# Kernel optimization log

Measured on AMD Instinct MI355X. Metric: run time of the kernel, lower is better.

## Reference

```python
import jax, jax.numpy as jnp
import numpy as np

N = 100000      # nodes
E = 1600000     # edges
F_IN, H1, H2, H3, F_OUT = 64, 128, 128, 64, 8


def _lin(key, fan_in, fan_out):
    return jax.random.normal(key, (fan_in, fan_out), jnp.float32) / np.sqrt(fan_in).astype(np.float32)


def setup_inputs() -> dict:
    key = jax.random.key(0)
    ks = jax.random.split(key, 16)
    x = jax.random.normal(ks[0], (N, F_IN), jnp.float32)
    edge_index = jax.random.randint(ks[1], (2, E), 0, N, dtype=jnp.int64)
    return {
        "x": x,
        "edge_index": edge_index,
        "eps1": jnp.zeros((), jnp.float32),
        "eps2": jnp.zeros((), jnp.float32),
        "eps3": jnp.zeros((), jnp.float32),
        "W1a": _lin(ks[2], F_IN, H1), "b1a": jnp.zeros((H1,), jnp.float32),
        "W1b": _lin(ks[3], H1, H1),   "b1b": jnp.zeros((H1,), jnp.float32),
        "W2a": _lin(ks[4], H1, H2),   "b2a": jnp.zeros((H2,), jnp.float32),
        "W2b": _lin(ks[5], H2, H2),   "b2b": jnp.zeros((H2,), jnp.float32),
        "W3a": _lin(ks[6], H2, H3),   "b3a": jnp.zeros((H3,), jnp.float32),
        "W3b": _lin(ks[7], H3, H3),   "b3b": jnp.zeros((H3,), jnp.float32),
        "Wfc": _lin(ks[8], H3, F_OUT), "bfc": jnp.zeros((F_OUT,), jnp.float32),
    }


def _gin_conv(x, src, dst, eps, Wa, ba, Wb, bb):
    # out_i = MLP((1+eps) * x_i + sum_{j in N(i)} x_j)
    agg = jax.ops.segment_sum(x[src], dst, num_segments=N)  # scatter-add over edges
    h = (1.0 + eps) * x + agg
    return jax.nn.relu(h @ Wa + ba) @ Wb + bb


def reference(x, edge_index, eps1, eps2, eps3,
              W1a, b1a, W1b, b1b,
              W2a, b2a, W2b, b2b,
              W3a, b3a, W3b, b3b,
              Wfc, bfc):
    src, dst = edge_index[0], edge_index[1]
    x = jax.nn.relu(_gin_conv(x, src, dst, eps1, W1a, b1a, W1b, b1b))
    x = jax.nn.relu(_gin_conv(x, src, dst, eps2, W2a, b2a, W2b, b2b))
    x = jax.nn.relu(_gin_conv(x, src, dst, eps3, W3a, b3a, W3b, b3b))
    emb = jax.lax.stop_gradient(x)  # x.clone().detach()
    out = x @ Wfc + bfc
    return out, emb
```

## Files before the change

kernel.cpp:

```cpp
#include <hip/hip_runtime.h>
#include <hip/hip_bf16.h>
#include <stdint.h>

typedef unsigned short ushort_t;
typedef __attribute__((ext_vector_type(8))) short short8;
typedef __attribute__((ext_vector_type(4))) float floatx4;
typedef __attribute__((ext_vector_type(2))) float floatx2;

__device__ __forceinline__ float bf2f(unsigned short u){
  union { unsigned int i; float f; } v; v.i = ((unsigned int)u) << 16; return v.f;
}
__device__ __forceinline__ unsigned short f2bf(float f){
  union { float f; unsigned int i; } v; v.f = f;
  unsigned int r = v.i + 0x7FFFu + ((v.i >> 16) & 1u);
  return (unsigned short)(r >> 16);
}
__device__ __forceinline__ unsigned int pack2(unsigned short lo, unsigned short hi){
  return ((unsigned int)hi << 16) | (unsigned int)lo;
}
__device__ __forceinline__ float bflo(unsigned int v){
  union { unsigned int u; float f; } c; c.u = v << 16; return c.f;
}
__device__ __forceinline__ float bfhi(unsigned int v){
  union { unsigned int u; float f; } c; c.u = v & 0xffff0000u; return c.f;
}
__device__ __forceinline__ floatx2 bfpair(unsigned int v){
  union { unsigned int u; float f; } lo, hi;
  lo.u = v << 16; hi.u = v & 0xffff0000u;
  floatx2 r; r.x = lo.f; r.y = hi.f; return r;
}


__global__ __launch_bounds__(256)
void k_prep(const unsigned int* __restrict__ w, int* __restrict__ ghist, int E, int N, int nbB,
            const float2* __restrict__ xin, unsigned int* __restrict__ xb, int total2, int tobfB,
            const float* __restrict__ W1a, const float* __restrict__ W1b, const float* __restrict__ W2a,
            const float* __restrict__ W2b, const float* __restrict__ W3a, const float* __restrict__ W3b,
            const float* __restrict__ Wfc, ushort_t* __restrict__ wout)
{
  int b = blockIdx.x, t = threadIdx.x;
  if (b < nbB){
    __shared__ int h[256];
    __shared__ unsigned int dred[4];
    h[t] = 0;
    int base = b*4096 + t;
    unsigned int acc = 0;
    #pragma unroll
    for (int i=0;i<16;++i){
      int e = base + i*256;
      if (e < E) acc |= w[2*e+1];
    }
    #pragma unroll
    for (int o=32;o>=1;o>>=1) acc |= __shfl_xor(acc, o);
    if ((t&63)==0) dred[t>>6] = acc;
    __syncthreads();
    int m = (dred[0]|dred[1]|dred[2]|dred[3]) != 0;
    #pragma unroll
    for (int i=0;i<16;++i){
      int e = base + i*256;
      if (e < E){
        int d = m ? (int)w[(size_t)E + e] : (int)w[2*((size_t)E + e)];
        if ((unsigned)d < (unsigned)N) atomicAdd(&h[d>>9], 1);
      }
    }
    __syncthreads();
    if (h[t]) atomicAdd(&ghist[t], h[t]);
  } else if (b < nbB + tobfB){
    int i = (b - nbB)*256 + t;
    if (i < total2){
      float2 v = xin[i];
      xb[i] = pack2(f2bf(v.x), f2bf(v.y));
    }
  } else {
    int id = (b - nbB - tobfB)*256 + t;
    const float* src; int K, M, base2, local;
    if      (id <  8192){ src=W1a; K=64;  M=128; base2=0;     local=id; }
    else if (id < 24576){ src=W1b; K=128; M=128; base2=8192;  local=id-8192; }
    else if (id < 40960){ src=W2a; K=128; M=128; base2=24576; local=id-24576; }
    else if (id < 57344){ src=W2b; K=128; M=128; base2=40960; local=id-40960; }
    else if (id < 65536){ src=W3a; K=128; M=64;  base2=57344; local=id-57344; }
    else if (id < 69632){ src=W3b; K=64;  M=64;  base2=65536; local=id-65536; }
    else if (id < 70656){ src=Wfc; K=64;  M=16;  base2=69632; local=id-69632; }
    else if (id < 74752){ src=nullptr; K=64; M=64; base2=70656; local=id-70656; }
    else return;
    int k = local / M, nn = local - k*M;
    float val;
    if (src == nullptr) val = (k == nn) ? 1.0f : 0.0f;
    else if (src == Wfc) val = (nn<8) ? Wfc[k*8+nn] : 0.0f;
    else                 val = src[k*M+nn];
    int idx = (((nn>>4)*(K/32) + (k>>5))*4 + ((k>>3)&3))*128 + (nn&15)*8 + (k&7);
    wout[base2+idx] = f2bf(val);
  }
}


__global__ __launch_bounds__(256) void k_bscan(const int* __restrict__ ghist, int* __restrict__ bbase,
                                               int* __restrict__ gcur, int NB){
  __shared__ int sv[256];
  int t = threadIdx.x;
  int v = (t < NB) ? ghist[t] : 0;
  sv[t] = v; __syncthreads();
  for (int o=1;o<256;o<<=1){
    int xv = (t>=o)? sv[t-o] : 0;
    __syncthreads();
    sv[t] += xv;
    __syncthreads();
  }
  int excl = sv[t] - v;
  if (t < NB){ bbase[t] = excl; gcur[t] = excl; }
  if (t == NB-1) bbase[NB] = excl + v;
}

__global__ __launch_bounds__(256) void k_bin(const unsigned int* __restrict__ w,
                                             int* __restrict__ gcur, int2* __restrict__ pairs,
                                             int E, int N, int NB){
  __shared__ int h[256];
  __shared__ int cur[256];
  __shared__ unsigned int dred[4];
  int t = threadIdx.x;
  h[t] = 0;
  int base = blockIdx.x*4096 + t;
  unsigned int acc = 0;
  #pragma unroll
  for (int i=0;i<16;++i){
    int e = base + i*256;
    if (e < E) acc |= w[2*e+1];
  }
  #pragma unroll
  for (int o=32;o>=1;o>>=1) acc |= __shfl_xor(acc, o);
  if ((t&63)==0) dred[t>>6] = acc;
  __syncthreads();
  int m = (dred[0]|dred[1]|dred[2]|dred[3]) != 0;
  int d[16], s[16];
  #pragma unroll
  for (int i=0;i<16;++i){
    int e = base + i*256;
    d[i] = -1; s[i] = 0;
    if (e < E){
      if (m){ s[i] = (int)w[e];           d[i] = (int)w[(size_t)E + e]; }
      else  { s[i] = (int)w[2*(size_t)e]; d[i] = (int)w[2*((size_t)E + e)]; }
      if ((unsigned)d[i] >= (unsigned)N || (unsigned)s[i] >= (unsigned)N) d[i] = -1;
    }
  }
  #pragma unroll
  for (int i=0;i<16;++i)
    if (d[i] >= 0) atomicAdd(&h[d[i]>>9], 1);
  __syncthreads();
  if (t < NB && h[t]) cur[t] = atomicAdd(&gcur[t], h[t]);
  __syncthreads();
  #pragma unroll
  for (int i=0;i<16;++i){
    if (d[i] >= 0){
      int p = atomicAdd(&cur[d[i]>>9], 1);
      pairs[p] = make_int2(d[i], s[i]);
    }
  }
}

__global__ __launch_bounds__(256) void k_bcsr(const int2* __restrict__ pairs, const int* __restrict__ bbase,
                                              int* __restrict__ offs, int* __restrict__ csr, int N, int NB){
  __shared__ int cnt[512];
  __shared__ int wsum[4];
  int b = blockIdx.x, t = threadIdx.x, lane = t&63, wv = t>>6;
  int lo = bbase[b], hi = bbase[b+1];
  int node0 = b << 9;
  cnt[t] = 0; cnt[t+256] = 0;
  __syncthreads();
  for (int i = lo+t; i < hi; i += 256){
    int2 p = pairs[i];
    atomicAdd(&cnt[p.x - node0], 1);
  }
  __syncthreads();
  int v0 = cnt[2*t], v1 = cnt[2*t+1], tot = v0+v1;
  int s = tot;
  #pragma unroll
  for (int o=1;o<64;o<<=1){ int xv = __shfl_up(s,o); if (lane>=o) s += xv; }
  if (lane==63) wsum[wv] = s;
  __syncthreads();
  int basev = 0;
  for (int j=0;j<wv;++j) basev += wsum[j];
  int excl = basev + s - tot;
  int e0 = lo + excl, e1 = lo + excl + v0;
  cnt[2*t] = e0; cnt[2*t+1] = e1;
  int n0 = node0 + 2*t, n1 = node0 + 2*t + 1;
  if (n0 < N) offs[n0] = e0;
  if (n1 < N) offs[n1] = e1;
  if (b == NB-1 && t == 255) offs[N] = hi;
  __syncthreads();
  for (int i = lo+t; i < hi; i += 256){
    int2 p = pairs[i];
    int pos = atomicAdd(&cnt[p.x - node0], 1);
    csr[pos] = p.y;
  }
}


template<int F>
__global__ __launch_bounds__(256) void k_gatherx(const uint4* __restrict__ xr, const int* __restrict__ offs,
                                                 const int* __restrict__ csr, const float* __restrict__ epsp,
                                                 uint4* __restrict__ hr, int n, int nzrow){
  constexpr int RS  = F/8;
  constexpr int LPN = 4*RS;
  constexpr int NPW = 64/LPN;
  constexpr int CH  = LPN;
  constexpr int MAXG = CH/16;
  int gt = blockIdx.x*256 + threadIdx.x;
  int wv = gt >> 6, lane = gt & 63;
  int grp = lane / LPN;
  int lin = lane % LPN;
  int q   = lin / RS;
  int f   = lin % RS;
  int node = wv*NPW + grp;
  if (node >= n) return;
  const size_t row = (size_t)node*RS;
  float e1s = 1.0f + epsp[0];
  floatx2 a0,a1,a2,a3;
  if (q == 0){
    uint4 sv = xr[row + f];
    floatx2 es; es.x = e1s; es.y = e1s;
    a0 = es*bfpair(sv.x); a1 = es*bfpair(sv.y);
    a2 = es*bfpair(sv.z); a3 = es*bfpair(sv.w);
  } else {
    floatx2 z; z.x = 0.f; z.y = 0.f;
    a0 = z; a1 = z; a2 = z; a3 = z;
  }
  int u0 = offs[node], u1 = offs[node+1];
  int deg = u1 - u0;

#define ISSUE(g, V0,V1,V2,V3) { int bb = grp*LPN + (g)*16 + q; \
    int s0=__shfl(cv,bb), s1=__shfl(cv,bb+4), s2=__shfl(cv,bb+8), s3=__shfl(cv,bb+12); \
    V0 = xr[(size_t)s0*RS + f]; V1 = xr[(size_t)s1*RS + f]; \
    V2 = xr[(size_t)s2*RS + f]; V3 = xr[(size_t)s3*RS + f]; }
#define ACCV(V)  { a0 += bfpair((V).x); a1 += bfpair((V).y); a2 += bfpair((V).z); a3 += bfpair((V).w); }
#define ACC4(V0,V1,V2,V3) { ACCV(V0) ACCV(V1) ACCV(V2) ACCV(V3) }

  for (int c0 = 0; c0 < deg; c0 += CH){
    int rem = deg - c0;
    int cv = nzrow;
    if (lin < rem) cv = csr[u0 + c0 + lin];
    int nk = rem < CH ? rem : CH;
    int ng = (nk + 15) >> 4;
    uint4 A0,A1,A2,A3, B0,B1,B2,B3;
    ISSUE(0, A0,A1,A2,A3)
    if (ng > 1) { ISSUE(1, B0,B1,B2,B3) }
    ACC4(A0,A1,A2,A3)
    if (ng > 1){
      if constexpr (MAXG >= 3) { if (ng > 2) ISSUE(2, A0,A1,A2,A3) }
      ACC4(B0,B1,B2,B3)
      if constexpr (MAXG >= 3){
        if (ng > 2){
          if (ng > 3) { ISSUE(3, B0,B1,B2,B3) }
          ACC4(A0,A1,A2,A3)
          if (ng > 3) { ACC4(B0,B1,B2,B3) }
        }
      }
    }
  }
#undef ISSUE
#undef ACCV
#undef ACC4
#define RED(av) { av.x += __shfl_xor(av.x, RS);   av.y += __shfl_xor(av.y, RS); \
                  av.x += __shfl_xor(av.x, 2*RS); av.y += __shfl_xor(av.y, 2*RS); }
  RED(a0) RED(a1) RED(a2) RED(a3)
#undef RED
  if (q == 0){
    uint4 o;
    o.x = pack2(f2bf(a0.x), f2bf(a0.y));
    o.y = pack2(f2bf(a1.x), f2bf(a1.y));
    o.z = pack2(f2bf(a2.x), f2bf(a2.y));
    o.w = pack2(f2bf(a3.x), f2bf(a3.y));
    hr[row + f] = o;
  }
}


template<int F, int M1, int M2, bool LAST, bool Y3>
__global__ __launch_bounds__(256)
void k_mlp(const ushort_t* __restrict__ h,
           const ushort_t* __restrict__ wp1, const float* __restrict__ b1,
           const ushort_t* __restrict__ wp2, const float* __restrict__ b2,
           ushort_t* __restrict__ xout,
           float* __restrict__ embp,
           const ushort_t* __restrict__ wpfc, const float* __restrict__ bfc,
           float* __restrict__ outp, int n)
{
  constexpr int NT1 = M1/16, NT2 = M2/16, KC1 = F/32, KC2 = M1/32;
  __shared__ short sC1[4*(M1/8)*136];
  __shared__ short sX3[LAST ? (4*8*136) : 1];
  int tid = threadIdx.x, lane = tid&63, w = tid>>6;
  int m16 = lane&15, quad = lane>>4;
  int row0 = blockIdx.x*64 + w*16;
  size_t arow = (size_t)(row0 + m16);

  floatx4 acc[NT1];
  #pragma unroll
  for (int i=0;i<NT1;++i) acc[i] = (floatx4){0.f,0.f,0.f,0.f};
  #pragma unroll
  for (int kc=0; kc<KC1; ++kc){
    short8 a = *(const short8*)(h + arow*F + kc*32 + quad*8);
    #pragma unroll
    for (int nt=0; nt<NT1; ++nt){
      short8 b = *(const short8*)(wp1 + (size_t)((nt*KC1+kc)*64 + lane)*8);
      acc[nt] = __builtin_amdgcn_mfma_f32_16x16x32_bf16(a, b, acc[nt], 0, 0, 0);
    }
  }
  #pragma unroll
  for (int nt=0; nt<NT1; ++nt){
    int c = nt*16 + m16;
    float bias = b1[c];
    #pragma unroll
    for (int r=0;r<4;++r){
      float v = fmaxf(acc[nt][r] + bias, 0.f);
      int mm = quad*4 + r;
      sC1[(w*(M1/8) + (c>>3))*136 + mm*8 + (c&7)] = (short)f2bf(v);
    }
  }
  __syncthreads();

  floatx4 acc2[NT2];
  #pragma unroll
  for (int i=0;i<NT2;++i) acc2[i] = (floatx4){0.f,0.f,0.f,0.f};
  #pragma unroll
  for (int kc=0; kc<KC2; ++kc){
    short8 a = *(const short8*)&sC1[(w*(M1/8) + kc*4 + quad)*136 + m16*8];
    #pragma unroll
    for (int nt=0; nt<NT2; ++nt){
      short8 b = *(const short8*)(wp2 + (size_t)((nt*KC2+kc)*64 + lane)*8);
      acc2[nt] = __builtin_amdgcn_mfma_f32_16x16x32_bf16(a, b, acc2[nt], 0, 0, 0);
    }
  }
  #pragma unroll
  for (int nt=0; nt<NT2; ++nt){
    int c = nt*16 + m16;
    float bias = b2[c];
    #pragma unroll
    for (int r=0;r<4;++r){
      float v = fmaxf(acc2[nt][r] + bias, 0.f);
      int mm = quad*4 + r;
      int row = row0 + mm;
      if constexpr (Y3){
        sC1[(w*(M2/8) + (c>>3))*136 + mm*8 + (c&7)] = (short)f2bf(v);
      } else if constexpr (!LAST){
        if (row < n) xout[(size_t)row*M2 + c] = f2bf(v);
      } else {
        if (row < n) embp[(size_t)row*64 + c] = v;
        sX3[(w*8 + (c>>3))*136 + mm*8 + (c&7)] = (short)f2bf(v);
      }
    }
  }

  if constexpr (Y3){
    constexpr int KC3 = M2/32;
    floatx4 acc3[4];
    #pragma unroll
    for (int i=0;i<4;++i) acc3[i] = (floatx4){0.f,0.f,0.f,0.f};
    #pragma unroll
    for (int kc=0; kc<KC3; ++kc){
      short8 a = *(const short8*)&sC1[(w*(M2/8) + kc*4 + quad)*136 + m16*8];
      #pragma unroll
      for (int nt=0; nt<4; ++nt){
        short8 b = *(const short8*)(wpfc + (size_t)((nt*KC3+kc)*64 + lane)*8);
        acc3[nt] = __builtin_amdgcn_mfma_f32_16x16x32_bf16(a, b, acc3[nt], 0, 0, 0);
      }
    }
    #pragma unroll
    for (int nt=0; nt<4; ++nt){
      int c = nt*16 + m16;
      #pragma unroll
      for (int r=0;r<4;++r){
        int row = row0 + quad*4 + r;
        if (row < n) xout[(size_t)row*64 + c] = f2bf(acc3[nt][r]);
      }
    }
  }

  if constexpr (LAST){
    __syncthreads();
    floatx4 accf = (floatx4){0.f,0.f,0.f,0.f};
    #pragma unroll
    for (int kc=0; kc<2; ++kc){
      short8 a = *(const short8*)&sX3[(w*8 + kc*4 + quad)*136 + m16*8];
      short8 b = *(const short8*)(wpfc + (size_t)(kc*64 + lane)*8);
      accf = __builtin_amdgcn_mfma_f32_16x16x32_bf16(a, b, accf, 0, 0, 0);
    }
    if (m16 < 8){
      float bias = bfc[m16];
      #pragma unroll
      for (int r=0;r<4;++r){
        int row = row0 + quad*4 + r;
        if (row < n) outp[(size_t)row*8 + m16] = accf[r] + bias;
      }
    }
  }
}


extern "C" void kernel_launch(void* const* d_in, const int* in_sizes, int n_in,
                              void* d_out, int out_size, void* d_ws, size_t ws_size,
                              hipStream_t stream)
{
  const int N = in_sizes[0] / 64;
  const int E = in_sizes[1] / 2;
  const int NB = (N + 511) / 512;
  const float*        x    = (const float*)d_in[0];
  const unsigned int* ew   = (const unsigned int*)d_in[1];
  const float* eps1 = (const float*)d_in[2];
  const float* eps2 = (const float*)d_in[3];
  const float* eps3 = (const float*)d_in[4];
  const float* W1a  = (const float*)d_in[5];
  const float* b1a  = (const float*)d_in[6];
  const float* W1b  = (const float*)d_in[7];
  const float* b1b  = (const float*)d_in[8];
  const float* W2a  = (const float*)d_in[9];
  const float* b2a  = (const float*)d_in[10];
  const float* W2b  = (const float*)d_in[11];
  const float* b2b  = (const float*)d_in[12];
  const float* W3a  = (const float*)d_in[13];
  const float* b3a  = (const float*)d_in[14];
  const float* W3b  = (const float*)d_in[15];
  const float* b3b  = (const float*)d_in[16];
  const float* Wfc  = (const float*)d_in[17];
  const float* bfc  = (const float*)d_in[18];

  float* outp = (float*)d_out;
  float* emb  = outp + (size_t)N*8;

  const int Npad = ((N + 63)/64)*64;

  char* ws = (char*)d_ws;
  size_t o = 0;
  auto alloc = [&](size_t bytes)->char* {
    char* p = ws + o;
    o = (o + bytes + 255) & ~(size_t)255;
    return p;
  };
  int*      ghist = (int*)alloc(256*4);
  int*      bbase = (int*)alloc(257*4);
  int*      gcur  = (int*)alloc(256*4);
  int*      offs  = (int*)alloc((size_t)(N+1)*4);
  int2*     pairs = (int2*)alloc((size_t)E*8);
  int*      csr   = (int*)alloc((size_t)E*4);
  ushort_t* wperm = (ushort_t*)alloc(74752ull*2);
  ushort_t* xb    = (ushort_t*)alloc(((size_t)Npad + 64)*64*2);
  ushort_t* hbuf  = (ushort_t*)alloc((size_t)Npad*128*2);
  ushort_t* x1    = (ushort_t*)alloc(((size_t)Npad + 64)*128*2);
  ushort_t* ybuf  = (ushort_t*)alloc(((size_t)Npad + 64)*64*2);

  hipMemsetAsync(ghist, 0, 256*4, stream);
  hipMemsetAsync(xb + (size_t)N*64, 0, 64*2, stream);
  hipMemsetAsync(x1 + (size_t)N*128, 0, 128*2, stream);
  hipMemsetAsync(ybuf + (size_t)N*64, 0, 64*2, stream);
  const int nbB   = (E + 4095)/4096;
  const int tobfB = (N*32 + 255)/256;
  const int permB = 74752/256;
  k_prep<<<nbB + tobfB + permB, 256, 0, stream>>>(ew, ghist, E, N, nbB,
                                                  (const float2*)x, (unsigned int*)xb, N*32, tobfB,
                                                  W1a, W1b, W2a, W2b, W3a, W3b, Wfc, wperm);
  k_bscan<<<1, 256, 0, stream>>>(ghist, bbase, gcur, NB);
  k_bin<<<nbB, 256, 0, stream>>>(ew, gcur, pairs, E, N, NB);
  k_bcsr<<<NB, 256, 0, stream>>>(pairs, bbase, offs, csr, N, NB);

  k_gatherx<64><<<(N+7)/8, 256, 0, stream>>>((const uint4*)xb, offs, csr, eps1,
                                             (uint4*)hbuf, N, N);
  k_mlp<64,128,128,false,false><<<Npad/64, 256, 0, stream>>>(hbuf, wperm+0, b1a, wperm+8192, b1b,
                                                             x1, nullptr, nullptr, nullptr, nullptr, N);
  k_gatherx<128><<<(N+3)/4, 256, 0, stream>>>((const uint4*)x1, offs, csr, eps2,
                                              (uint4*)hbuf, N, N);
  k_mlp<128,128,128,false,true><<<Npad/64, 256, 0, stream>>>(hbuf, wperm+24576, b2a, wperm+40960, b2b,
                                                             ybuf, nullptr, wperm+57344, nullptr, nullptr, N);
  k_gatherx<64><<<(N+7)/8, 256, 0, stream>>>((const uint4*)ybuf, offs, csr, eps3,
                                             (uint4*)hbuf, N, N);
  k_mlp<64,64,64,true,false><<<Npad/64, 256, 0, stream>>>(hbuf, wperm+70656, b3a, wperm+65536, b3b,
                                                          nullptr, emb, wperm+69632, bfc, outp, N);
}
```

Baseline: 358.8 us.

## Store layer-1 output in feature slices and gather each slice separately

The first MLP now writes its 128-wide output as 8 slices of 16 features, each a separate (N+1)x16 array. A new gather kernel processes one slice per block group, so concurrently running blocks touch a 3.2MB slice that is more likely to stay in cache during the random neighbour gathers. The zero padding row for each slice is written inside the prep kernel instead of a memset. The cost is more gather blocks, re-reading the CSR once per slice, and scattered 2-byte stores in the MLP epilogue.

Result: slower. 379.9 us (+5.9%).

```diff
diff --git a/kernel.cpp b/kernel.cpp
--- a/kernel.cpp
+++ b/kernel.cpp
@@ -36,7 +36,8 @@
             const float2* __restrict__ xin, unsigned int* __restrict__ xb, int total2, int tobfB,
             const float* __restrict__ W1a, const float* __restrict__ W1b, const float* __restrict__ W2a,
             const float* __restrict__ W2b, const float* __restrict__ W3a, const float* __restrict__ W3b,
-            const float* __restrict__ Wfc, ushort_t* __restrict__ wout)
+            const float* __restrict__ Wfc, ushort_t* __restrict__ wout,
+            ushort_t* __restrict__ x1z, int ssx1)
 {
   int b = blockIdx.x, t = threadIdx.x;
   if (b < nbB){
@@ -73,6 +74,12 @@
     }
   } else {
     int id = (b - nbB - tobfB)*256 + t;
+    if (id >= 74752){
+      int id2 = id - 74752;
+      if (id2 < 128)
+        x1z[(size_t)(id2>>4)*ssx1 + (size_t)N*16 + (id2&15)] = 0;
+      return;
+    }
     const float* src; int K, M, base2, local;
     if      (id <  8192){ src=W1a; K=64;  M=128; base2=0;     local=id; }
     else if (id < 24576){ src=W1b; K=128; M=128; base2=8192;  local=id-8192; }
@@ -81,8 +88,7 @@
     else if (id < 65536){ src=W3a; K=128; M=64;  base2=57344; local=id-57344; }
     else if (id < 69632){ src=W3b; K=64;  M=64;  base2=65536; local=id-65536; }
     else if (id < 70656){ src=Wfc; K=64;  M=16;  base2=69632; local=id-69632; }
-    else if (id < 74752){ src=nullptr; K=64; M=64; base2=70656; local=id-70656; }
-    else return;
+    else                { src=nullptr; K=64; M=64; base2=70656; local=id-70656; }
     int k = local / M, nn = local - k*M;
     float val;
     if (src == nullptr) val = (k == nn) ? 1.0f : 0.0f;
@@ -274,7 +280,55 @@
 }
 
 
-template<int F, int M1, int M2, bool LAST, bool Y3>
+__global__ __launch_bounds__(256)
+void k_gslice(const ushort_t* __restrict__ xs, const int* __restrict__ offs,
+              const int* __restrict__ csr, const float* __restrict__ epsp,
+              uint4* __restrict__ hr, int n, int ss)
+{
+  int bid = blockIdx.x;
+  int s  = bid & 7, nb = bid >> 3;
+  int t = threadIdx.x, wv = t >> 6, lane = t & 63;
+  int nd = lane >> 3, l8 = lane & 7, pair = l8 >> 1, half = l8 & 1;
+  int node = nb*32 + wv*8 + nd;
+  if (node >= n) return;
+  const uint4* p = (const uint4*)(xs + (size_t)s*ss);
+  float e1s = 1.0f + epsp[0];
+  floatx2 a0,a1,a2,a3;
+  { floatx2 z; z.x=0.f; z.y=0.f; a0=z; a1=z; a2=z; a3=z; }
+  if (pair == 0){
+    uint4 sv = p[(size_t)node*2 + half];
+    floatx2 es; es.x=e1s; es.y=e1s;
+    a0 = es*bfpair(sv.x); a1 = es*bfpair(sv.y); a2 = es*bfpair(sv.z); a3 = es*bfpair(sv.w);
+  }
+  int u0 = offs[node], u1 = offs[node+1];
+  int deg = u1 - u0;
+  for (int c0 = 0; c0 < deg; c0 += 8){
+    int rem = deg - c0;
+    int cv = n;
+    if (l8 < rem) cv = csr[u0 + c0 + l8];
+    int s0 = __shfl(cv, nd*8 + pair);
+    int s1 = __shfl(cv, nd*8 + 4 + pair);
+    uint4 V0 = p[(size_t)s0*2 + half];
+    uint4 V1 = p[(size_t)s1*2 + half];
+    a0 += bfpair(V0.x); a1 += bfpair(V0.y); a2 += bfpair(V0.z); a3 += bfpair(V0.w);
+    a0 += bfpair(V1.x); a1 += bfpair(V1.y); a2 += bfpair(V1.z); a3 += bfpair(V1.w);
+  }
+#define RED2(av) { av.x += __shfl_xor(av.x, 2); av.y += __shfl_xor(av.y, 2); \
+                   av.x += __shfl_xor(av.x, 4); av.y += __shfl_xor(av.y, 4); }
+  RED2(a0) RED2(a1) RED2(a2) RED2(a3)
+#undef RED2
+  if (pair == 0){
+    uint4 o;
+    o.x = pack2(f2bf(a0.x), f2bf(a0.y));
+    o.y = pack2(f2bf(a1.x), f2bf(a1.y));
+    o.z = pack2(f2bf(a2.x), f2bf(a2.y));
+    o.w = pack2(f2bf(a3.x), f2bf(a3.y));
+    hr[(size_t)node*16 + s*2 + half] = o;
+  }
+}
+
+
+template<int F, int M1, int M2, bool LAST, bool Y3, bool SLICEOUT>
 __global__ __launch_bounds__(256)
 void k_mlp(const ushort_t* __restrict__ h,
            const ushort_t* __restrict__ wp1, const float* __restrict__ b1,
@@ -282,7 +336,7 @@
            ushort_t* __restrict__ xout,
            float* __restrict__ embp,
            const ushort_t* __restrict__ wpfc, const float* __restrict__ bfc,
-           float* __restrict__ outp, int n)
+           float* __restrict__ outp, int n, int ss)
 {
   constexpr int NT1 = M1/16, NT2 = M2/16, KC1 = F/32, KC2 = M1/32;
   __shared__ short sC1[4*(M1/8)*136];
@@ -340,6 +394,8 @@
       int row = row0 + mm;
       if constexpr (Y3){
         sC1[(w*(M2/8) + (c>>3))*136 + mm*8 + (c&7)] = (short)f2bf(v);
+      } else if constexpr (SLICEOUT){
+        if (row < n) xout[(size_t)nt*ss + (size_t)row*16 + m16] = f2bf(v);
       } else if constexpr (!LAST){
         if (row < n) xout[(size_t)row*M2 + c] = f2bf(v);
       } else {
@@ -426,6 +482,7 @@
   float* emb  = outp + (size_t)N*8;
 
   const int Npad = ((N + 63)/64)*64;
+  const int ssx1 = (N + 1) * 16;
 
   char* ws = (char*)d_ws;
   size_t o = 0;
@@ -443,33 +500,32 @@
   ushort_t* wperm = (ushort_t*)alloc(74752ull*2);
   ushort_t* xb    = (ushort_t*)alloc(((size_t)Npad + 64)*64*2);
   ushort_t* hbuf  = (ushort_t*)alloc((size_t)Npad*128*2);
-  ushort_t* x1    = (ushort_t*)alloc(((size_t)Npad + 64)*128*2);
+  ushort_t* x1    = (ushort_t*)alloc((size_t)8*ssx1*2);
   ushort_t* ybuf  = (ushort_t*)alloc(((size_t)Npad + 64)*64*2);
 
   hipMemsetAsync(ghist, 0, 256*4, stream);
   hipMemsetAsync(xb + (size_t)N*64, 0, 64*2, stream);
-  hipMemsetAsync(x1 + (size_t)N*128, 0, 128*2, stream);
   hipMemsetAsync(ybuf + (size_t)N*64, 0, 64*2, stream);
   const int nbB   = (E + 4095)/4096;
   const int tobfB = (N*32 + 255)/256;
-  const int permB = 74752/256;
+  const int permB = (74752 + 128 + 255)/256;
   k_prep<<<nbB + tobfB + permB, 256, 0, stream>>>(ew, ghist, E, N, nbB,
                                                   (const float2*)x, (unsigned int*)xb, N*32, tobfB,
-                                                  W1a, W1b, W2a, W2b, W3a, W3b, Wfc, wperm);
+                                                  W1a, W1b, W2a, W2b, W3a, W3b, Wfc, wperm,
+                                                  x1, ssx1);
   k_bscan<<<1, 256, 0, stream>>>(ghist, bbase, gcur, NB);
   k_bin<<<nbB, 256, 0, stream>>>(ew, gcur, pairs, E, N, NB);
   k_bcsr<<<NB, 256, 0, stream>>>(pairs, bbase, offs, csr, N, NB);
 
   k_gatherx<64><<<(N+7)/8, 256, 0, stream>>>((const uint4*)xb, offs, csr, eps1,
                                              (uint4*)hbuf, N, N);
-  k_mlp<64,128,128,false,false><<<Npad/64, 256, 0, stream>>>(hbuf, wperm+0, b1a, wperm+8192, b1b,
-                                                             x1, nullptr, nullptr, nullptr, nullptr, N);
-  k_gatherx<128><<<(N+3)/4, 256, 0, stream>>>((const uint4*)x1, offs, csr, eps2,
-                                              (uint4*)hbuf, N, N);
-  k_mlp<128,128,128,false,true><<<Npad/64, 256, 0, stream>>>(hbuf, wperm+24576, b2a, wperm+40960, b2b,
-                                                             ybuf, nullptr, wperm+57344, nullptr, nullptr, N);
+  k_mlp<64,128,128,false,false,true><<<Npad/64, 256, 0, stream>>>(hbuf, wperm+0, b1a, wperm+8192, b1b,
+                                                                  x1, nullptr, nullptr, nullptr, nullptr, N, ssx1);
+  k_gslice<<<((N+31)/32)*8, 256, 0, stream>>>(x1, offs, csr, eps2, (uint4*)hbuf, N, ssx1);
+  k_mlp<128,128,128,false,true,false><<<Npad/64, 256, 0, stream>>>(hbuf, wperm+24576, b2a, wperm+40960, b2b,
+                                                                   ybuf, nullptr, wperm+57344, nullptr, nullptr, N, 0);
   k_gatherx<64><<<(N+7)/8, 256, 0, stream>>>((const uint4*)ybuf, offs, csr, eps3,
                                              (uint4*)hbuf, N, N);
-  k_mlp<64,64,64,true,false><<<Npad/64, 256, 0, stream>>>(hbuf, wperm+70656, b3a, wperm+65536, b3b,
-                                                          nullptr, emb, wperm+69632, bfc, outp, N);
-}
+  k_mlp<64,64,64,true,false,false><<<Npad/64, 256, 0, stream>>>(hbuf, wperm+70656, b3a, wperm+65536, b3b,
+                                                                nullptr, emb, wperm+69632, bfc, outp, N, 0);
+}
```

## Fuse neighbor gather into MLP kernels for layers 1 and 3, drop scan kernel

Applied to the files above, without the earlier changes.

Layers 1 and 3 (64-wide features) now use a new kernel that performs the neighbour aggregation for a 64-node tile directly into shared memory and then runs the two-layer MFMA MLP. This removes the intermediate hbuf write and read and one launch per fused layer. The block-offset scan is recomputed redundantly inside k_bin and k_bcsr, so the separate k_bscan launch goes away. The pad-row memsets are folded into k_prep. The trade-off is lower gather parallelism per block and extra shared memory, which may reduce occupancy.

After: 360.5 us. Within noise of the previous version (+0.5%).

```diff
diff --git a/kernel.cpp b/kernel.cpp
--- a/kernel.cpp
+++ b/kernel.cpp
@@ -7,9 +7,6 @@
 typedef __attribute__((ext_vector_type(4))) float floatx4;
 typedef __attribute__((ext_vector_type(2))) float floatx2;
 
-__device__ __forceinline__ float bf2f(unsigned short u){
-  union { unsigned int i; float f; } v; v.i = ((unsigned int)u) << 16; return v.f;
-}
 __device__ __forceinline__ unsigned short f2bf(float f){
   union { float f; unsigned int i; } v; v.f = f;
   unsigned int r = v.i + 0x7FFFu + ((v.i >> 16) & 1u);
@@ -17,12 +14,6 @@
 }
 __device__ __forceinline__ unsigned int pack2(unsigned short lo, unsigned short hi){
   return ((unsigned int)hi << 16) | (unsigned int)lo;
-}
-__device__ __forceinline__ float bflo(unsigned int v){
-  union { unsigned int u; float f; } c; c.u = v << 16; return c.f;
-}
-__device__ __forceinline__ float bfhi(unsigned int v){
-  union { unsigned int u; float f; } c; c.u = v & 0xffff0000u; return c.f;
 }
 __device__ __forceinline__ floatx2 bfpair(unsigned int v){
   union { unsigned int u; float f; } lo, hi;
@@ -36,7 +27,8 @@
             const float2* __restrict__ xin, unsigned int* __restrict__ xb, int total2, int tobfB,
             const float* __restrict__ W1a, const float* __restrict__ W1b, const float* __restrict__ W2a,
             const float* __restrict__ W2b, const float* __restrict__ W3a, const float* __restrict__ W3b,
-            const float* __restrict__ Wfc, ushort_t* __restrict__ wout)
+            const float* __restrict__ Wfc, ushort_t* __restrict__ wout,
+            ushort_t* __restrict__ xbz, ushort_t* __restrict__ x1z, ushort_t* __restrict__ ybz)
 {
   int b = blockIdx.x, t = threadIdx.x;
   if (b < nbB){
@@ -73,6 +65,13 @@
     }
   } else {
     int id = (b - nbB - tobfB)*256 + t;
+    if (id >= 74752){
+      int id2 = id - 74752;
+      if      (id2 <  64) xbz[id2]      = 0;
+      else if (id2 < 192) x1z[id2-64]   = 0;
+      else if (id2 < 256) ybz[id2-192]  = 0;
+      return;
+    }
     const float* src; int K, M, base2, local;
     if      (id <  8192){ src=W1a; K=64;  M=128; base2=0;     local=id; }
     else if (id < 24576){ src=W1b; K=128; M=128; base2=8192;  local=id-8192; }
@@ -81,8 +80,7 @@
     else if (id < 65536){ src=W3a; K=128; M=64;  base2=57344; local=id-57344; }
     else if (id < 69632){ src=W3b; K=64;  M=64;  base2=65536; local=id-65536; }
     else if (id < 70656){ src=Wfc; K=64;  M=16;  base2=69632; local=id-69632; }
-    else if (id < 74752){ src=nullptr; K=64; M=64; base2=70656; local=id-70656; }
-    else return;
+    else                { src=nullptr; K=64; M=64; base2=70656; local=id-70656; }
     int k = local / M, nn = local - k*M;
     float val;
     if (src == nullptr) val = (k == nn) ? 1.0f : 0.0f;
@@ -94,30 +92,25 @@
 }
 
 
-__global__ __launch_bounds__(256) void k_bscan(const int* __restrict__ ghist, int* __restrict__ bbase,
-                                               int* __restrict__ gcur, int NB){
+__global__ __launch_bounds__(256) void k_bin(const unsigned int* __restrict__ w,
+                                             const int* __restrict__ ghist, int* __restrict__ gcur,
+                                             int2* __restrict__ pairs,
+                                             int E, int N, int NB){
   __shared__ int sv[256];
-  int t = threadIdx.x;
-  int v = (t < NB) ? ghist[t] : 0;
-  sv[t] = v; __syncthreads();
-  for (int o=1;o<256;o<<=1){
-    int xv = (t>=o)? sv[t-o] : 0;
-    __syncthreads();
-    sv[t] += xv;
-    __syncthreads();
-  }
-  int excl = sv[t] - v;
-  if (t < NB){ bbase[t] = excl; gcur[t] = excl; }
-  if (t == NB-1) bbase[NB] = excl + v;
-}
-
-__global__ __launch_bounds__(256) void k_bin(const unsigned int* __restrict__ w,
-                                             int* __restrict__ gcur, int2* __restrict__ pairs,
-                                             int E, int N, int NB){
   __shared__ int h[256];
   __shared__ int cur[256];
   __shared__ unsigned int dred[4];
   int t = threadIdx.x;
+  int gv = ghist[t];
+  sv[t] = gv; __syncthreads();
+  for (int o=1;o<256;o<<=1){
+    int xv = (t>=o)? sv[t-o] : 0;
+    __syncthreads();
+    sv[t] += xv;
+    __syncthreads();
+  }
+  int excl = sv[t] - gv;
+
   h[t] = 0;
   int base = blockIdx.x*4096 + t;
   unsigned int acc = 0;
@@ -146,7 +139,7 @@
   for (int i=0;i<16;++i)
     if (d[i] >= 0) atomicAdd(&h[d[i]>>9], 1);
   __syncthreads();
-  if (t < NB && h[t]) cur[t] = atomicAdd(&gcur[t], h[t]);
+  if (t < NB && h[t]) cur[t] = excl + atomicAdd(&gcur[t], h[t]);
   __syncthreads();
   #pragma unroll
   for (int i=0;i<16;++i){
@@ -157,12 +150,22 @@
   }
 }
 
-__global__ __launch_bounds__(256) void k_bcsr(const int2* __restrict__ pairs, const int* __restrict__ bbase,
+__global__ __launch_bounds__(256) void k_bcsr(const int2* __restrict__ pairs, const int* __restrict__ ghist,
                                               int* __restrict__ offs, int* __restrict__ csr, int N, int NB){
+  __shared__ int sv[256];
   __shared__ int cnt[512];
   __shared__ int wsum[4];
   int b = blockIdx.x, t = threadIdx.x, lane = t&63, wv = t>>6;
-  int lo = bbase[b], hi = bbase[b+1];
+  int gv = ghist[t];
+  sv[t] = gv; __syncthreads();
+  for (int o=1;o<256;o<<=1){
+    int xv = (t>=o)? sv[t-o] : 0;
+    __syncthreads();
+    sv[t] += xv;
+    __syncthreads();
+  }
+  int lo = (b==0) ? 0 : sv[b-1];
+  int hi = sv[b];
   int node0 = b << 9;
   cnt[t] = 0; cnt[t+256] = 0;
   __syncthreads();
@@ -276,6 +279,210 @@
 
 template<int F, int M1, int M2, bool LAST, bool Y3>
 __global__ __launch_bounds__(256)
+void k_gmlp(const uint4* __restrict__ xr, const int* __restrict__ offs,
+            const int* __restrict__ csr, const float* __restrict__ epsp,
+            const ushort_t* __restrict__ wp1, const float* __restrict__ b1,
+            const ushort_t* __restrict__ wp2, const float* __restrict__ b2,
+            ushort_t* __restrict__ xout,
+            float* __restrict__ embp,
+            const ushort_t* __restrict__ wpfc, const float* __restrict__ bfc,
+            float* __restrict__ outp, int n)
+{
+  constexpr int RS  = F/8;
+  constexpr int LPN = 4*RS;
+  constexpr int NPW = 64/LPN;
+  constexpr int CH  = LPN;
+  constexpr int MAXG = CH/16;
+  constexpr int NPR = 4*NPW;
+  constexpr int PADC = F + 8;
+  constexpr int NT1 = M1/16, NT2 = M2/16, KC1 = F/32, KC2 = M1/32;
+
+  __shared__ short sH[64*PADC] __attribute__((aligned(16)));
+  __shared__ short sC1[4*(M1/8)*136];
+  __shared__ short sX3[LAST ? (4*8*136) : 1];
+
+  int tid = threadIdx.x, lane = tid&63, w = tid>>6;
+  int node0 = blockIdx.x*64;
+
+  {
+    int grp = lane / LPN;
+    int lin = lane % LPN;
+    int q   = lin / RS;
+    int f   = lin % RS;
+    float e1s = 1.0f + epsp[0];
+    #pragma unroll
+    for (int rd = 0; rd < 64/NPR; ++rd){
+      int lrow = rd*NPR + w*NPW + grp;
+      int node = node0 + lrow;
+      int nd = node < n ? node : n;
+      floatx2 a0,a1,a2,a3;
+      if (q == 0){
+        uint4 sv = xr[(size_t)nd*RS + f];
+        floatx2 es; es.x = e1s; es.y = e1s;
+        a0 = es*bfpair(sv.x); a1 = es*bfpair(sv.y);
+        a2 = es*bfpair(sv.z); a3 = es*bfpair(sv.w);
+      } else {
+        floatx2 z; z.x = 0.f; z.y = 0.f;
+        a0 = z; a1 = z; a2 = z; a3 = z;
+      }
+      int u0 = 0, deg = 0;
+      if (node < n){ u0 = offs[node]; deg = offs[node+1] - u0; }
+
+#define ISSUE(g, V0,V1,V2,V3) { int bb = grp*LPN + (g)*16 + q; \
+    int s0=__shfl(cv,bb), s1=__shfl(cv,bb+4), s2=__shfl(cv,bb+8), s3=__shfl(cv,bb+12); \
+    V0 = xr[(size_t)s0*RS + f]; V1 = xr[(size_t)s1*RS + f]; \
+    V2 = xr[(size_t)s2*RS + f]; V3 = xr[(size_t)s3*RS + f]; }
+#define ACCV(V)  { a0 += bfpair((V).x); a1 += bfpair((V).y); a2 += bfpair((V).z); a3 += bfpair((V).w); }
+#define ACC4(V0,V1,V2,V3) { ACCV(V0) ACCV(V1) ACCV(V2) ACCV(V3) }
+      for (int c0 = 0; c0 < deg; c0 += CH){
+        int rem = deg - c0;
+        int cv = n;
+        if (lin < rem) cv = csr[u0 + c0 + lin];
+        int nk = rem < CH ? rem : CH;
+        int ng = (nk + 15) >> 4;
+        uint4 A0,A1,A2,A3, B0,B1,B2,B3;
+        ISSUE(0, A0,A1,A2,A3)
+        if (ng > 1) { ISSUE(1, B0,B1,B2,B3) }
+        ACC4(A0,A1,A2,A3)
+        if (ng > 1){
+          if constexpr (MAXG >= 3) { if (ng > 2) ISSUE(2, A0,A1,A2,A3) }
+          ACC4(B0,B1,B2,B3)
+          if constexpr (MAXG >= 3){
+            if (ng > 2){
+              if (ng > 3) { ISSUE(3, B0,B1,B2,B3) }
+              ACC4(A0,A1,A2,A3)
+              if (ng > 3) { ACC4(B0,B1,B2,B3) }
+            }
+          }
+        }
+      }
+#undef ISSUE
+#undef ACCV
+#undef ACC4
+#define RED(av) { av.x += __shfl_xor(av.x, RS);   av.y += __shfl_xor(av.y, RS); \
+                  av.x += __shfl_xor(av.x, 2*RS); av.y += __shfl_xor(av.y, 2*RS); }
+      RED(a0) RED(a1) RED(a2) RED(a3)
+#undef RED
+      if (q == 0){
+        uint4 o;
+        o.x = pack2(f2bf(a0.x), f2bf(a0.y));
+        o.y = pack2(f2bf(a1.x), f2bf(a1.y));
+        o.z = pack2(f2bf(a2.x), f2bf(a2.y));
+        o.w = pack2(f2bf(a3.x), f2bf(a3.y));
+        *(uint4*)&sH[lrow*PADC + f*8] = o;
+      }
+    }
+  }
+  __syncthreads();
+
+  int m16 = lane&15, quad = lane>>4;
+  int row0 = node0 + w*16;
+
+  floatx4 acc[NT1];
+  #pragma unroll
+  for (int i=0;i<NT1;++i) acc[i] = (floatx4){0.f,0.f,0.f,0.f};
+  #pragma unroll
+  for (int kc=0; kc<KC1; ++kc){
+    short8 a = *(const short8*)&sH[(w*16 + m16)*PADC + kc*32 + quad*8];
+    #pragma unroll
+    for (int nt=0; nt<NT1; ++nt){
+      short8 b = *(const short8*)(wp1 + (size_t)((nt*KC1+kc)*64 + lane)*8);
+      acc[nt] = __builtin_amdgcn_mfma_f32_16x16x32_bf16(a, b, acc[nt], 0, 0, 0);
+    }
+  }
+  #pragma unroll
+  for (int nt=0; nt<NT1; ++nt){
+    int c = nt*16 + m16;
+    float bias = b1[c];
+    #pragma unroll
+    for (int r=0;r<4;++r){
+      float v = fmaxf(acc[nt][r] + bias, 0.f);
+      int mm = quad*4 + r;
+      sC1[(w*(M1/8) + (c>>3))*136 + mm*8 + (c&7)] = (short)f2bf(v);
+    }
+  }
+  __syncthreads();
+
+  floatx4 acc2[NT2];
+  #pragma unroll
+  for (int i=0;i<NT2;++i) acc2[i] = (floatx4){0.f,0.f,0.f,0.f};
+  #pragma unroll
+  for (int kc=0; kc<KC2; ++kc){
+    short8 a = *(const short8*)&sC1[(w*(M1/8) + kc*4 + quad)*136 + m16*8];
+    #pragma unroll
+    for (int nt=0; nt<NT2; ++nt){
+      short8 b = *(const short8*)(wp2 + (size_t)((nt*KC2+kc)*64 + lane)*8);
+      acc2[nt] = __builtin_amdgcn_mfma_f32_16x16x32_bf16(a, b, acc2[nt], 0, 0, 0);
+    }
+  }
+  #pragma unroll
+  for (int nt=0; nt<NT2; ++nt){
+    int c = nt*16 + m16;
+    float bias = b2[c];
+    #pragma unroll
+    for (int r=0;r<4;++r){
+      float v = fmaxf(acc2[nt][r] + bias, 0.f);
+      int mm = quad*4 + r;
+      int row = row0 + mm;
+      if constexpr (Y3){
+        sC1[(w*(M2/8) + (c>>3))*136 + mm*8 + (c&7)] = (short)f2bf(v);
+      } else if constexpr (!LAST){
+        if (row < n) xout[(size_t)row*M2 + c] = f2bf(v);
+      } else {
+        if (row < n) embp[(size_t)row*64 + c] = v;
+        sX3[(w*8 + (c>>3))*136 + mm*8 + (c&7)] = (short)f2bf(v);
+      }
+    }
+  }
+
+  if constexpr (Y3){
+    constexpr int KC3 = M2/32;
+    floatx4 acc3[4];
+    #pragma unroll
+    for (int i=0;i<4;++i) acc3[i] = (floatx4){0.f,0.f,0.f,0.f};
+    #pragma unroll
+    for (int kc=0; kc<KC3; ++kc){
+      short8 a = *(const short8*)&sC1[(w*(M2/8) + kc*4 + quad)*136 + m16*8];
+      #pragma unroll
+      for (int nt=0; nt<4; ++nt){
+        short8 b = *(const short8*)(wpfc + (size_t)((nt*KC3+kc)*64 + lane)*8);
+        acc3[nt] = __builtin_amdgcn_mfma_f32_16x16x32_bf16(a, b, acc3[nt], 0, 0, 0);
+      }
+    }
+    #pragma unroll
+    for (int nt=0; nt<4; ++nt){
+      int c = nt*16 + m16;
+      #pragma unroll
+      for (int r=0;r<4;++r){
+        int row = row0 + quad*4 + r;
+        if (row < n) xout[(size_t)row*64 + c] = f2bf(acc3[nt][r]);
+      }
+    }
+  }
+
+  if constexpr (LAST){
+    __syncthreads();
+    floatx4 accf = (floatx4){0.f,0.f,0.f,0.f};
+    #pragma unroll
+    for (int kc=0; kc<2; ++kc){
+      short8 a = *(const short8*)&sX3[(w*8 + kc*4 + quad)*136 + m16*8];
+      short8 b = *(const short8*)(wpfc + (size_t)(kc*64 + lane)*8);
+      accf = __builtin_amdgcn_mfma_f32_16x16x32_bf16(a, b, accf, 0, 0, 0);
+    }
+    if (m16 < 8){
+      float bias = bfc[m16];
+      #pragma unroll
+      for (int r=0;r<4;++r){
+        int row = row0 + quad*4 + r;
+        if (row < n) outp[(size_t)row*8 + m16] = accf[r] + bias;
+      }
+    }
+  }
+}
+
+
+template<int F, int M1, int M2, bool LAST, bool Y3>
+__global__ __launch_bounds__(256)
 void k_mlp(const ushort_t* __restrict__ h,
            const ushort_t* __restrict__ wp1, const float* __restrict__ b1,
            const ushort_t* __restrict__ wp2, const float* __restrict__ b2,
@@ -434,9 +641,8 @@
     o = (o + bytes + 255) & ~(size_t)255;
     return p;
   };
-  int*      ghist = (int*)alloc(256*4);
-  int*      bbase = (int*)alloc(257*4);
-  int*      gcur  = (int*)alloc(256*4);
+  int*      ghist = (int*)alloc(512*4);
+  int*      gcur  = ghist + 256;
   int*      offs  = (int*)alloc((size_t)(N+1)*4);
   int2*     pairs = (int2*)alloc((size_t)E*8);
   int*      csr   = (int*)alloc((size_t)E*4);
@@ -446,30 +652,25 @@
   ushort_t* x1    = (ushort_t*)alloc(((size_t)Npad + 64)*128*2);
   ushort_t* ybuf  = (ushort_t*)alloc(((size_t)Npad + 64)*64*2);
 
-  hipMemsetAsync(ghist, 0, 256*4, stream);
-  hipMemsetAsync(xb + (size_t)N*64, 0, 64*2, stream);
-  hipMemsetAsync(x1 + (size_t)N*128, 0, 128*2, stream);
-  hipMemsetAsync(ybuf + (size_t)N*64, 0, 64*2, stream);
+  hipMemsetAsync(ghist, 0, 512*4, stream);
   const int nbB   = (E + 4095)/4096;
   const int tobfB = (N*32 + 255)/256;
-  const int permB = 74752/256;
+  const int permB = (74752 + 256 + 255)/256;
   k_prep<<<nbB + tobfB + permB, 256, 0, stream>>>(ew, ghist, E, N, nbB,
                                                   (const float2*)x, (unsigned int*)xb, N*32, tobfB,
-                                                  W1a, W1b, W2a, W2b, W3a, W3b, Wfc, wperm);
-  k_bscan<<<1, 256, 0, stream>>>(ghist, bbase, gcur, NB);
-  k_bin<<<nbB, 256, 0, stream>>>(ew, gcur, pairs, E, N, NB);
-  k_bcsr<<<NB, 256, 0, stream>>>(pairs, bbase, offs, csr, N, NB);
-
-  k_gatherx<64><<<(N+7)/8, 256, 0, stream>>>((const uint4*)xb, offs, csr, eps1,
-                                             (uint4*)hbuf, N, N);
-  k_mlp<64,128,128,false,false><<<Npad/64, 256, 0, stream>>>(hbuf, wperm+0, b1a, wperm+8192, b1b,
-                                                             x1, nullptr, nullptr, nullptr, nullptr, N);
+                                                  W1a, W1b, W2a, W2b, W3a, W3b, Wfc, wperm,
+                                                  xb + (size_t)N*64, x1 + (size_t)N*128, ybuf + (size_t)N*64);
+  k_bin<<<nbB, 256, 0, stream>>>(ew, ghist, gcur, pairs, E, N, NB);
+  k_bcsr<<<NB, 256, 0, stream>>>(pairs, ghist, offs, csr, N, NB);
+
+  k_gmlp<64,128,128,false,false><<<Npad/64, 256, 0, stream>>>((const uint4*)xb, offs, csr, eps1,
+                                                              wperm+0, b1a, wperm+8192, b1b,
+                                                              x1, nullptr, nullptr, nullptr, nullptr, N);
   k_gatherx<128><<<(N+3)/4, 256, 0, stream>>>((const uint4*)x1, offs, csr, eps2,
                                               (uint4*)hbuf, N, N);
   k_mlp<128,128,128,false,true><<<Npad/64, 256, 0, stream>>>(hbuf, wperm+24576, b2a, wperm+40960, b2b,
                                                              ybuf, nullptr, wperm+57344, nullptr, nullptr, N);
-  k_gatherx<64><<<(N+7)/8, 256, 0, stream>>>((const uint4*)ybuf, offs, csr, eps3,
-                                             (uint4*)hbuf, N, N);
-  k_mlp<64,64,64,true,false><<<Npad/64, 256, 0, stream>>>(hbuf, wperm+70656, b3a, wperm+65536, b3b,
-                                                          nullptr, emb, wperm+69632, bfc, outp, N);
-}
+  k_gmlp<64,64,64,true,false><<<Npad/64, 256, 0, stream>>>((const uint4*)ybuf, offs, csr, eps3,
+                                                           wperm+70656, b3a, wperm+65536, b3b,
+                                                           nullptr, emb, wperm+69632, bfc, outp, N);
+}
```
